# Kernel tuning notes

Measured on AMD Instinct MI355X. Metric: run time of the kernel, lower is better.

Reference implementation:

```python
import math
import jax, jax.numpy as jnp
import numpy as np

NUM_ATTENTION_MASK = 50
SCALE_FACTOR = 50.0


def setup_inputs() -> dict:
    key = jax.random.key(0)
    k1, k2, k3 = jax.random.split(key, 3)
    B, N = 16, NUM_ATTENTION_MASK
    # decoded boxes (x, y, w, h): centers land inside the 256x256 feature map
    xy = jax.random.uniform(k1, (B, N, 2), minval=0.0, maxval=200.0)
    wh = jax.random.uniform(k2, (B, N, 2), minval=10.0, maxval=60.0)
    boxes = jnp.concatenate([xy, wh], axis=-1)  # [B, N, 4]
    labels = jax.random.randint(k3, (B, N, 1), 0, 80).astype(jnp.float32)
    return {"boxes": boxes, "labels": labels, "fms_h": 256, "fms_w": 256}


def _channel_shuffle_perm(n_channels: int, groups: int) -> np.ndarray:
    # nn.ChannelShuffle: view (g, c/g) -> transpose -> flatten
    return np.arange(n_channels).reshape(groups, n_channels // groups).T.reshape(-1)


def reference(boxes, labels, fms_h, fms_w):
    B, N, _ = boxes.shape
    x, y, w, h = boxes[..., 0], boxes[..., 1], boxes[..., 2], boxes[..., 3]
    # xc = x + w // 2 (python floor-div on floats)
    xc = x + jnp.floor(w / 2.0)  # [B, N]
    yc = y + jnp.floor(h / 2.0)

    # grid coordinates: round(linspace(0, H, H)) as in MaskGenerator
    gx = jnp.round(jnp.linspace(0.0, fms_h, fms_h))  # [H]
    gy = jnp.round(jnp.linspace(0.0, fms_w, fms_w))  # [W]

    # Gaussian with covariance diag(0.25*w, 0.25*h):
    # quad[b,n,i,j] = (gx[i]-xc)^2/(0.25w) + (gy[j]-yc)^2/(0.25h)
    dx2 = (gx[None, None, :] - xc[..., None]) ** 2 / (0.25 * w)[..., None]  # [B,N,H]
    dy2 = (gy[None, None, :] - yc[..., None]) ** 2 / (0.25 * h)[..., None]  # [B,N,W]
    quad = dx2[..., :, None] + dy2[..., None, :]  # [B,N,H,W]

    det = 0.0625 * w * h  # det(diag(0.25w, 0.25h))
    factor1 = (2.0 * math.pi) ** (-1.0) * det ** (-0.5)  # [B,N]
    masks = factor1[..., None, None] * jnp.exp(-0.5 * quad)  # [B,N,H,W]

    # per-sample min-max normalize over (channel, H, W), then scale
    mn = masks.min(axis=(1, 2, 3), keepdims=True)
    mx = masks.max(axis=(1, 2, 3), keepdims=True)
    masks = (masks - mn) / (mx - mn) * SCALE_FACTOR

    # ChannelShuffle(groups = N // 2) on channel dim
    perm = _channel_shuffle_perm(N, N // 2)
    attention_masks = masks[:, perm]  # [B,N,H,W]
    attention_labels = jnp.squeeze(labels, -1)[:, perm]  # [B,N]
    return attention_masks, attention_labels
```

## Files before the change

kernel.cpp:

```cpp
#include <hip/hip_runtime.h>
#include <hip/hip_bf16.h>

#define NB 16
#define NN 50
#define HW 256

__device__ __forceinline__ float gridc(int i) { return (float)(i + (i >= 128 ? 1 : 0)); }

__device__ __forceinline__ float wredmax(float v) {
#pragma unroll
  for (int o = 32; o > 0; o >>= 1) v = fmaxf(v, __shfl_xor(v, o));
  return v;
}
__device__ __forceinline__ float wredmin(float v) {
#pragma unroll
  for (int o = 32; o > 0; o >>= 1) v = fminf(v, __shfl_xor(v, o));
  return v;
}

__global__ void k_minmax(const float* __restrict__ boxes, float2* __restrict__ mm) {
  int bn = blockIdx.x;
  float4 box = reinterpret_cast<const float4*>(boxes)[bn];
  float xc = box.x + floorf(box.z * 0.5f);
  float yc = box.y + floorf(box.w * 0.5f);
  int t = threadIdx.x;
  float g = gridc(t);
  float dx = g - xc, dy = g - yc;
  float ex = expf(-0.5f * (dx * dx) / (0.25f * box.z));
  float ey = expf(-0.5f * (dy * dy) / (0.25f * box.w));
  float exmx = wredmax(ex), exmn = wredmin(ex);
  float eymx = wredmax(ey), eymn = wredmin(ey);
  __shared__ float red[4][4];
  int wid = t >> 6;
  if ((t & 63) == 0) { red[wid][0] = exmx; red[wid][1] = exmn; red[wid][2] = eymx; red[wid][3] = eymn; }
  __syncthreads();
  if (t == 0) {
    float a = red[0][0], b2 = red[0][1], c = red[0][2], d = red[0][3];
#pragma unroll
    for (int k = 1; k < 4; ++k) {
      a = fmaxf(a, red[k][0]); b2 = fminf(b2, red[k][1]);
      c = fmaxf(c, red[k][2]); d = fminf(d, red[k][3]);
    }
    float det = 0.0625f * box.z * box.w;
    float f1 = 0.15915494309189535f / sqrtf(det);
    mm[bn] = make_float2(f1 * b2 * d, f1 * a * c);
  }
}

__global__ void k_batch(const float2* __restrict__ mm, const float* __restrict__ labels,
                        float2* __restrict__ bp, float* __restrict__ out_labels) {
  int b = blockIdx.x;
  int t = threadIdx.x;
  float mn = INFINITY, mx = -INFINITY;
  if (t < NN) { float2 v = mm[b * NN + t]; mn = v.x; mx = v.y; }
#pragma unroll
  for (int o = 32; o > 0; o >>= 1) {
    mn = fminf(mn, __shfl_xor(mn, o));
    mx = fmaxf(mx, __shfl_xor(mx, o));
  }
  if (t == 0) {
    float s = 50.0f / (mx - mn);
    bp[b] = make_float2(s, mn * s);
  }
  if (t < NN) {
    int src = (t < 25) ? 2 * t : 2 * (t - 25) + 1;
    out_labels[b * NN + t] = labels[b * NN + src];
  }
}

__global__ void k_masks(const float* __restrict__ boxes, const float2* __restrict__ bp,
                        float* __restrict__ out) {
  int blk = blockIdx.x;
  int tile = blk & 3;
  int bk = blk >> 2;
  int b = bk / NN;
  int k = bk - b * NN;
  int n = (k < 25) ? 2 * k : 2 * (k - 25) + 1;
  float4 box = reinterpret_cast<const float4*>(boxes)[b * NN + n];
  float xc = box.x + floorf(box.z * 0.5f);
  float yc = box.y + floorf(box.w * 0.5f);
  float2 p = bp[b];
  float s = p.x, mns = p.y;
  float det = 0.0625f * box.z * box.w;
  float A = (0.15915494309189535f / sqrtf(det)) * s;

  __shared__ float eyL[HW];
  __shared__ float exL[64];
  int t = threadIdx.x;
  {
    float g = gridc(t);
    float d = g - yc;
    eyL[t] = expf(-0.5f * (d * d) / (0.25f * box.w));
  }
  int row0 = tile * 64;
  if (t < 64) {
    float g = gridc(row0 + t);
    float d = g - xc;
    exL[t] = A * expf(-0.5f * (d * d) / (0.25f * box.z));
  }
  __syncthreads();

  int lane_col = (t & 63) * 4;
  int rsub = t >> 6;
  float eyr[4];
#pragma unroll
  for (int c = 0; c < 4; ++c) eyr[c] = eyL[lane_col + c];

  float* base = out + (size_t)bk * (HW * HW) + (size_t)row0 * HW;
#pragma unroll
  for (int it = 0; it < 16; ++it) {
    int r = rsub + it * 4;
    float coef = exL[r];
    float4 v;
    v.x = fmaf(coef, eyr[0], -mns);
    v.y = fmaf(coef, eyr[1], -mns);
    v.z = fmaf(coef, eyr[2], -mns);
    v.w = fmaf(coef, eyr[3], -mns);
    *reinterpret_cast<float4*>(base + r * HW + lane_col) = v;
  }
}

extern "C" void kernel_launch(void* const* d_in, const int* in_sizes, int n_in,
                              void* d_out, int out_size, void* d_ws, size_t ws_size,
                              hipStream_t stream) {
  const float* boxes = (const float*)d_in[0];
  const float* labels = (const float*)d_in[1];
  float* out = (float*)d_out;

  float2* mm = (float2*)d_ws;
  float2* bp = (float2*)((char*)d_ws + NB * NN * sizeof(float2));

  k_minmax<<<NB * NN, 256, 0, stream>>>(boxes, mm);
  k_batch<<<NB, 64, 0, stream>>>(mm, labels, bp, out + (size_t)NB * NN * HW * HW);
  k_masks<<<NB * NN * 4, 256, 0, stream>>>(boxes, bp, out);
}
```

Measured before the change: 39.55 us.

## Fuse min/max reduction into mask kernel using analytic per-box extrema

```diff
diff --git a/kernel.cpp b/kernel.cpp
--- a/kernel.cpp
+++ b/kernel.cpp
@@ -7,68 +7,13 @@
 
 __device__ __forceinline__ float gridc(int i) { return (float)(i + (i >= 128 ? 1 : 0)); }
 
-__device__ __forceinline__ float wredmax(float v) {
-#pragma unroll
-  for (int o = 32; o > 0; o >>= 1) v = fmaxf(v, __shfl_xor(v, o));
-  return v;
-}
-__device__ __forceinline__ float wredmin(float v) {
-#pragma unroll
-  for (int o = 32; o > 0; o >>= 1) v = fminf(v, __shfl_xor(v, o));
-  return v;
+__device__ __forceinline__ float nearest_grid(float c) {
+  float r = rintf(c);
+  if (r == 128.0f) r = (c < 128.0f) ? 127.0f : 129.0f;
+  return r;
 }
 
-__global__ void k_minmax(const float* __restrict__ boxes, float2* __restrict__ mm) {
-  int bn = blockIdx.x;
-  float4 box = reinterpret_cast<const float4*>(boxes)[bn];
-  float xc = box.x + floorf(box.z * 0.5f);
-  float yc = box.y + floorf(box.w * 0.5f);
-  int t = threadIdx.x;
-  float g = gridc(t);
-  float dx = g - xc, dy = g - yc;
-  float ex = expf(-0.5f * (dx * dx) / (0.25f * box.z));
-  float ey = expf(-0.5f * (dy * dy) / (0.25f * box.w));
-  float exmx = wredmax(ex), exmn = wredmin(ex);
-  float eymx = wredmax(ey), eymn = wredmin(ey);
-  __shared__ float red[4][4];
-  int wid = t >> 6;
-  if ((t & 63) == 0) { red[wid][0] = exmx; red[wid][1] = exmn; red[wid][2] = eymx; red[wid][3] = eymn; }
-  __syncthreads();
-  if (t == 0) {
-    float a = red[0][0], b2 = red[0][1], c = red[0][2], d = red[0][3];
-#pragma unroll
-    for (int k = 1; k < 4; ++k) {
-      a = fmaxf(a, red[k][0]); b2 = fminf(b2, red[k][1]);
-      c = fmaxf(c, red[k][2]); d = fminf(d, red[k][3]);
-    }
-    float det = 0.0625f * box.z * box.w;
-    float f1 = 0.15915494309189535f / sqrtf(det);
-    mm[bn] = make_float2(f1 * b2 * d, f1 * a * c);
-  }
-}
-
-__global__ void k_batch(const float2* __restrict__ mm, const float* __restrict__ labels,
-                        float2* __restrict__ bp, float* __restrict__ out_labels) {
-  int b = blockIdx.x;
-  int t = threadIdx.x;
-  float mn = INFINITY, mx = -INFINITY;
-  if (t < NN) { float2 v = mm[b * NN + t]; mn = v.x; mx = v.y; }
-#pragma unroll
-  for (int o = 32; o > 0; o >>= 1) {
-    mn = fminf(mn, __shfl_xor(mn, o));
-    mx = fmaxf(mx, __shfl_xor(mx, o));
-  }
-  if (t == 0) {
-    float s = 50.0f / (mx - mn);
-    bp[b] = make_float2(s, mn * s);
-  }
-  if (t < NN) {
-    int src = (t < 25) ? 2 * t : 2 * (t - 25) + 1;
-    out_labels[b * NN + t] = labels[b * NN + src];
-  }
-}
-
-__global__ void k_masks(const float* __restrict__ boxes, const float2* __restrict__ bp,
+__global__ void k_fused(const float* __restrict__ boxes, const float* __restrict__ labels,
                         float* __restrict__ out) {
   int blk = blockIdx.x;
   int tile = blk & 3;
@@ -76,17 +21,54 @@
   int b = bk / NN;
   int k = bk - b * NN;
   int n = (k < 25) ? 2 * k : 2 * (k - 25) + 1;
-  float4 box = reinterpret_cast<const float4*>(boxes)[b * NN + n];
+
+  const float4* boxes4 = reinterpret_cast<const float4*>(boxes);
+  int t = threadIdx.x;
+
+  __shared__ float sS, sMns;
+  float mn = INFINITY, mx = -INFINITY;
+  if (t < NN) {
+    float4 bx = boxes4[b * NN + t];
+    float xc = bx.x + floorf(bx.z * 0.5f);
+    float yc = bx.y + floorf(bx.w * 0.5f);
+    float gnx = nearest_grid(xc), gfx = (xc > 128.0f) ? 0.0f : 256.0f;
+    float gny = nearest_grid(yc), gfy = (yc > 128.0f) ? 0.0f : 256.0f;
+    float dnx = gnx - xc, dfx = gfx - xc, dny = gny - yc, dfy = gfy - yc;
+    float exmx = expf(-0.5f * (dnx * dnx) / (0.25f * bx.z));
+    float exmn = expf(-0.5f * (dfx * dfx) / (0.25f * bx.z));
+    float eymx = expf(-0.5f * (dny * dny) / (0.25f * bx.w));
+    float eymn = expf(-0.5f * (dfy * dfy) / (0.25f * bx.w));
+    float det = 0.0625f * bx.z * bx.w;
+    float f1 = 0.15915494309189535f / sqrtf(det);
+    mn = f1 * exmn * eymn;
+    mx = f1 * exmx * eymx;
+  }
+  if (t < 64) {
+#pragma unroll
+    for (int o = 32; o > 0; o >>= 1) {
+      mn = fminf(mn, __shfl_xor(mn, o));
+      mx = fmaxf(mx, __shfl_xor(mx, o));
+    }
+    if (t == 0) {
+      float s = 50.0f / (mx - mn);
+      sS = s;
+      sMns = mn * s;
+    }
+  }
+
+  if (k == 0 && tile == 0 && t < NN) {
+    int src = (t < 25) ? 2 * t : 2 * (t - 25) + 1;
+    out[(size_t)NB * NN * HW * HW + b * NN + t] = labels[b * NN + src];
+  }
+
+  float4 box = boxes4[b * NN + n];
   float xc = box.x + floorf(box.z * 0.5f);
   float yc = box.y + floorf(box.w * 0.5f);
-  float2 p = bp[b];
-  float s = p.x, mns = p.y;
   float det = 0.0625f * box.z * box.w;
-  float A = (0.15915494309189535f / sqrtf(det)) * s;
+  float f1 = 0.15915494309189535f / sqrtf(det);
 
   __shared__ float eyL[HW];
   __shared__ float exL[64];
-  int t = threadIdx.x;
   {
     float g = gridc(t);
     float d = g - yc;
@@ -96,9 +78,12 @@
   if (t < 64) {
     float g = gridc(row0 + t);
     float d = g - xc;
-    exL[t] = A * expf(-0.5f * (d * d) / (0.25f * box.z));
+    exL[t] = expf(-0.5f * (d * d) / (0.25f * box.z));
   }
   __syncthreads();
+
+  float A = f1 * sS;
+  float mns = sMns;
 
   int lane_col = (t & 63) * 4;
   int rsub = t >> 6;
@@ -110,7 +95,7 @@
 #pragma unroll
   for (int it = 0; it < 16; ++it) {
     int r = rsub + it * 4;
-    float coef = exL[r];
+    float coef = A * exL[r];
     float4 v;
     v.x = fmaf(coef, eyr[0], -mns);
     v.y = fmaf(coef, eyr[1], -mns);
@@ -126,11 +111,5 @@
   const float* boxes = (const float*)d_in[0];
   const float* labels = (const float*)d_in[1];
   float* out = (float*)d_out;
-
-  float2* mm = (float2*)d_ws;
-  float2* bp = (float2*)((char*)d_ws + NB * NN * sizeof(float2));
-
-  k_minmax<<<NB * NN, 256, 0, stream>>>(boxes, mm);
-  k_batch<<<NB, 64, 0, stream>>>(mm, labels, bp, out + (size_t)NB * NN * HW * HW);
-  k_masks<<<NB * NN * 4, 256, 0, stream>>>(boxes, bp, out);
+  k_fused<<<NB * NN * 4, 256, 0, stream>>>(boxes, labels, out);
 }
```

Result: faster. 33.05 us (-16.4%).
